# Kernel optimization log

Measured on AMD Instinct MI355X. Metric: run time of the kernel, lower is better.

## Reference

```python
import jax, jax.numpy as jnp
import numpy as np

N_DEST, N_SRC = 8192, 8192
FEAT, TFD, EMB, HID, HEADS = 1024, 256, 64, 128, 2
NEG_INF = -9e15


def setup_inputs() -> dict:
    key = jax.random.key(0)
    ks = jax.random.split(key, 8)
    bias = (jax.random.uniform(ks[0], (N_DEST, N_SRC)) < 0.01).astype(jnp.float32)
    emb_dest = jax.random.normal(ks[1], (N_DEST, EMB), jnp.float32)
    emb_src = jax.random.normal(ks[2], (N_SRC, EMB), jnp.float32)
    feature_src = jax.random.normal(ks[3], (N_SRC, FEAT), jnp.float32)
    scale = 0.05
    fc_W = jax.random.normal(ks[4], (TFD, FEAT), jnp.float32) * scale
    fc_b = jnp.zeros((TFD,), jnp.float32)
    dec_W = jax.random.normal(ks[5], (FEAT, TFD), jnp.float32) * scale
    dec_b = jnp.zeros((FEAT,), jnp.float32)
    att_W = jax.random.normal(ks[6], (HEADS, EMB, HID), jnp.float32) * scale
    att_W2 = jax.random.normal(ks[7], (HEADS, HID, HID), jnp.float32) * scale
    return dict(bias=bias, emb_dest=emb_dest, emb_src=emb_src,
                feature_src=feature_src, fc_W=fc_W, fc_b=fc_b,
                dec_W=dec_W, dec_b=dec_b, att_W=att_W, att_W2=att_W2)


def reference(bias, emb_dest, emb_src, feature_src, fc_W, fc_b, dec_W, dec_b, att_W, att_W2):
    # encoder: [N_src, FEAT] -> [N_src, TFD]
    transformed = feature_src @ fc_W.T + fc_b
    # per-head projections of node embeddings: h = emb @ W  -> [H, N, HID]
    h_src = jnp.einsum('ne,hed->hnd', emb_src, att_W)
    h_dst = jnp.einsum('me,hed->hmd', emb_dest, att_W)
    # e = elu((h_dst @ W2) @ h_src^T)  -> [H, N_dest, N_src]
    scores = jax.nn.elu(jnp.einsum('hmd,hdk,hnk->hmn', h_dst, att_W2, h_src))
    masked = jnp.where(bias > 0, scores, NEG_INF)
    attn = jax.nn.softmax(masked, axis=-1)  # row-wise over source nodes
    # aggregate transformed source features, mean over heads -> [N_dest, TFD]
    feature_src_re = jnp.einsum('hmn,nf->hmf', attn, transformed).mean(axis=0)
    # decoder (autoencoder reconstruction): [N_src, FEAT]
    feature_hat = transformed @ dec_W.T + dec_b
    return feature_src_re, feature_hat
```

## Files before the change

### kernel.cpp

```cpp
#include <hip/hip_runtime.h>
#include <hip/hip_bf16.h>

#define N_DEST 8192
#define N_SRC  8192
#define FEATD  1024
#define TFDIM  256
#define EMBD   64
#define HIDD   128
#define LDO    1024
#define SCAP 240
#define BMW  128

typedef float  f32x4  __attribute__((ext_vector_type(4)));
typedef __bf16 bf16x8 __attribute__((ext_vector_type(8)));
typedef unsigned short u16x4 __attribute__((ext_vector_type(4)));

__device__ inline bf16x8 load8cvt(const float* p) {
  const f32x4 u = *(const f32x4*)p;
  const f32x4 v = *(const f32x4*)(p + 4);
  bf16x8 r;
  #pragma unroll
  for (int i = 0; i < 4; ++i) { r[i] = (__bf16)u[i]; r[i + 4] = (__bf16)v[i]; }
  return r;
}
__device__ inline unsigned short bfbits(float f) {
  __bf16 b = (__bf16)f;
  return *(unsigned short*)&b;
}
__device__ inline float bf2f(unsigned short u) {
  union { unsigned int i; float f; } x;
  x.i = (unsigned int)u << 16;
  return x.f;
}

__global__ __launch_bounds__(256) void cvt_weights(
    const float* __restrict__ fc_W, const float* __restrict__ dec_W,
    unsigned short* __restrict__ wpack, unsigned short* __restrict__ dpack)
{
  const int which = blockIdx.x >> 8;
  const int i = ((blockIdx.x & 255) * 256 + threadIdx.x) * 4;
  const float* src = which ? dec_W : fc_W;
  unsigned short* dst = which ? dpack : wpack;
  const f32x4 v = *(const f32x4*)(src + i);
  u16x4 o;
  #pragma unroll
  for (int e = 0; e < 4; ++e) o[e] = bfbits(v[e]);
  *(u16x4*)(dst + i) = o;
}

__global__ __launch_bounds__(256) void bias_to_bits(
    const float* __restrict__ bias, unsigned long long* __restrict__ bm)
{
  const int m = blockIdx.x;
  const int tid = threadIdx.x, lane = tid & 63, wv = tid >> 6;
  const float* brow = bias + (size_t)m * N_SRC;
  unsigned long long* bmrow = bm + (size_t)m * BMW;
  #pragma unroll
  for (int k = 0; k < 8; ++k) {
    const f32x4 v = *(const f32x4*)(brow + k * 1024 + tid * 4);
    #pragma unroll
    for (int e = 0; e < 4; ++e) {
      const unsigned long long msk = __ballot(v[e] > 0.f);
      if (lane == 0) bmrow[k * 16 + wv * 4 + e] = msk;
    }
  }
}

__global__ __launch_bounds__(256) void gemm_mfma_k1(
    const float* __restrict__ A, const float* __restrict__ B,
    const float* __restrict__ bias, float* __restrict__ stage,
    unsigned short* __restrict__ apack,
    const unsigned short* __restrict__ wpack)
{
  const int wave = threadIdx.x >> 6, lane = threadIdx.x & 63;
  const int l15 = lane & 15, quad = lane >> 4;
  const int row0 = blockIdx.x * 64 + wave * 16;
  const int col0 = blockIdx.y * 64;

  const float* Ap = A + (size_t)(row0 + l15) * FEATD + quad * 8;

  f32x4 acc[4];
  #pragma unroll
  for (int i = 0; i < 4; ++i) acc[i] = (f32x4){0.f, 0.f, 0.f, 0.f};

  if (wpack) {
    const unsigned short* Bq = wpack + (size_t)(col0 + l15) * FEATD + quad * 8;
    for (int k = 0; k < FEATD; k += 32) {
      const bf16x8 a  = load8cvt(Ap + k);
      const bf16x8 b0 = *(const bf16x8*)(Bq + k);
      const bf16x8 b1 = *(const bf16x8*)(Bq + (size_t)16 * FEATD + k);
      const bf16x8 b2 = *(const bf16x8*)(Bq + (size_t)32 * FEATD + k);
      const bf16x8 b3 = *(const bf16x8*)(Bq + (size_t)48 * FEATD + k);
      acc[0] = __builtin_amdgcn_mfma_f32_16x16x32_bf16(a, b0, acc[0], 0, 0, 0);
      acc[1] = __builtin_amdgcn_mfma_f32_16x16x32_bf16(a, b1, acc[1], 0, 0, 0);
      acc[2] = __builtin_amdgcn_mfma_f32_16x16x32_bf16(a, b2, acc[2], 0, 0, 0);
      acc[3] = __builtin_amdgcn_mfma_f32_16x16x32_bf16(a, b3, acc[3], 0, 0, 0);
    }
  } else {
    const float* Bp = B + (size_t)(col0 + l15) * FEATD + quad * 8;
    for (int k = 0; k < FEATD; k += 32) {
      const bf16x8 a  = load8cvt(Ap + k);
      const bf16x8 b0 = load8cvt(Bp + k);
      const bf16x8 b1 = load8cvt(Bp + (size_t)16 * FEATD + k);
      const bf16x8 b2 = load8cvt(Bp + (size_t)32 * FEATD + k);
      const bf16x8 b3 = load8cvt(Bp + (size_t)48 * FEATD + k);
      acc[0] = __builtin_amdgcn_mfma_f32_16x16x32_bf16(a, b0, acc[0], 0, 0, 0);
      acc[1] = __builtin_amdgcn_mfma_f32_16x16x32_bf16(a, b1, acc[1], 0, 0, 0);
      acc[2] = __builtin_amdgcn_mfma_f32_16x16x32_bf16(a, b2, acc[2], 0, 0, 0);
      acc[3] = __builtin_amdgcn_mfma_f32_16x16x32_bf16(a, b3, acc[3], 0, 0, 0);
    }
  }

  #pragma unroll
  for (int ct = 0; ct < 4; ++ct) {
    const int n = col0 + ct * 16 + l15;
    const float bn = bias[n];
    #pragma unroll
    for (int r = 0; r < 4; ++r) {
      const int mm = row0 + quad * 4 + r;
      const float v = acc[ct][r] + bn;
      stage[(size_t)mm * LDO + n] = v;
      if (apack) apack[(size_t)mm * TFDIM + n] = bfbits(v);
    }
  }
}

__global__ __launch_bounds__(128) void proj_all(
    const float* __restrict__ emb_src, const float* __restrict__ emb_dest,
    const float* __restrict__ att_W, const float* __restrict__ att_W2,
    float* __restrict__ stage, unsigned short* __restrict__ hpack)
{
  const int t = threadIdx.x;
  const int b = blockIdx.x;
  const int rb    = b & 511;
  const int h     = (b >> 9) & 1;
  const int which = b >> 10;
  const int row0  = rb * 16;

  __shared__ float se[16][EMBD];
  __shared__ float hh[16][HIDD];

  const float* e = (which ? emb_dest : emb_src) + (size_t)row0 * EMBD;
  for (int i = t; i < 16 * EMBD; i += 128) se[i >> 6][i & 63] = e[i];
  __syncthreads();

  float acc[16];
  #pragma unroll
  for (int r = 0; r < 16; ++r) acc[r] = 0.f;
  const float* W = att_W + (size_t)h * EMBD * HIDD + t;
  for (int d = 0; d < EMBD; ++d) {
    const float w = W[d * HIDD];
    #pragma unroll
    for (int r = 0; r < 16; ++r) acc[r] += se[r][d] * w;
  }

  if (!which) {
    #pragma unroll
    for (int r = 0; r < 16; ++r) {
      const size_t row = row0 + r;
      stage[row * LDO + 256 + h * HIDD + t] = acc[r];
      if (hpack) hpack[row * TFDIM + h * HIDD + t] = bfbits(acc[r]);
    }
    return;
  }

  #pragma unroll
  for (int r = 0; r < 16; ++r) hh[r][t] = acc[r];
  __syncthreads();

  float g[16];
  #pragma unroll
  for (int r = 0; r < 16; ++r) g[r] = 0.f;
  const float* W2 = att_W2 + (size_t)h * HIDD * HIDD + t;
  for (int d = 0; d < HIDD; ++d) {
    const float w2 = W2[d * HIDD];
    #pragma unroll
    for (int r = 0; r < 16; ++r) g[r] += hh[r][d] * w2;
  }
  #pragma unroll
  for (int r = 0; r < 16; ++r)
    stage[(size_t)(row0 + r) * LDO + 512 + h * HIDD + t] = g[r];
}

__global__ __launch_bounds__(256, 6) void attn_fused(
    const unsigned long long* __restrict__ bm, const float* __restrict__ stage,
    const unsigned short* __restrict__ hpack,
    const unsigned short* __restrict__ apack,
    float* __restrict__ out)
{
  const int m = blockIdx.x;
  const int tid = threadIdx.x;
  const int lane = tid & 63, wv = tid >> 6;

  __shared__ float gq[4][68];
  __shared__ unsigned long long bmw[BMW];
  __shared__ float s0[256], s1[256];
  __shared__ int   lidx[256];
  __shared__ float rA[4], rB[4];
  __shared__ float p0[4][TFDIM], p1[4][TFDIM];
  __shared__ int   cnt;

  const float* gs = stage + (size_t)m * LDO + 512;
  gq[wv][lane] = gs[(wv >> 1) * HIDD + (wv & 1) * 64 + lane];
  if (tid < BMW) bmw[tid] = bm[(size_t)m * BMW + tid];
  if (tid == 0) cnt = 0;
  __syncthreads();

  int wcount = 0;
  if (lane < 32) wcount = __popcll(bmw[(lane >> 2) * 16 + wv * 4 + (lane & 3)]);
  #pragma unroll
  for (int off = 32; off; off >>= 1) wcount += __shfl_xor(wcount, off);
  int wbase = 0;
  if (lane == 0) wbase = atomicAdd(&cnt, wcount);
  wbase = __shfl(wbase, 0);

  int off = wbase;
  #pragma unroll
  for (int k = 0; k < 8; ++k) {
    #pragma unroll
    for (int e = 0; e < 4; ++e) {
      const unsigned long long msk = bmw[k * 16 + wv * 4 + e];
      if ((msk >> lane) & 1ull) {
        const int p = off + __popcll(msk & ((1ull << lane) - 1ull));
        if (p < 256) lidx[p] = k * 1024 + wv * 256 + lane * 4 + e;
      }
      off += __popcll(msk);
    }
  }
  __syncthreads();
  const int count = cnt;

  if (count > 0 && count <= SCAP) {
    const int countPad = (count + 15) & ~15;
    if (tid >= count && tid < countPad) lidx[tid] = 0;
    __syncthreads();

    const int grp = tid >> 2, r4 = tid & 3;
    const int h = r4 >> 1, half = r4 & 1;
    const float* gh = gq[r4];
    for (int t0 = 0; t0 < count; t0 += 64) {
      const int t = t0 + grp;
      float q = 0.f;
      if (t < count) {
        const int j = lidx[t];
        const __bf16* hb =
            (const __bf16*)hpack + (size_t)j * TFDIM + h * HIDD + half * 64;
        #pragma unroll
        for (int s = 0; s < 8; ++s) {
          const bf16x8 x = *(const bf16x8*)(hb + s * 8);
          #pragma unroll
          for (int e = 0; e < 8; ++e) q += gh[s * 8 + e] * (float)x[e];
        }
      }
      q += __shfl_xor(q, 1);
      if (t < count && half == 0) {
        const float sc = (q > 0.f) ? q : expm1f(q);
        if (h == 0) s0[t] = sc; else s1[t] = sc;
      }
    }
    __syncthreads();

    float m0 = (tid < count) ? s0[tid] : -3.4e38f;
    float m1 = (tid < count) ? s1[tid] : -3.4e38f;
    #pragma unroll
    for (int o = 32; o; o >>= 1) {
      m0 = fmaxf(m0, __shfl_xor(m0, o));
      m1 = fmaxf(m1, __shfl_xor(m1, o));
    }
    if (lane == 0) { rA[wv] = m0; rB[wv] = m1; }
    __syncthreads();
    const float M0 = fmaxf(fmaxf(rA[0], rA[1]), fmaxf(rA[2], rA[3]));
    const float M1 = fmaxf(fmaxf(rB[0], rB[1]), fmaxf(rB[2], rB[3]));
    __syncthreads();

    float w0 = 0.f, w1 = 0.f;
    if (tid < count) {
      w0 = __expf(s0[tid] - M0);
      w1 = __expf(s1[tid] - M1);
    }
    if (tid < countPad) { s0[tid] = w0; s1[tid] = w1; }
    float l0 = w0, l1 = w1;
    #pragma unroll
    for (int o = 32; o; o >>= 1) {
      l0 += __shfl_xor(l0, o);
      l1 += __shfl_xor(l1, o);
    }
    if (lane == 0) { rA[wv] = l0; rB[wv] = l1; }
    __syncthreads();
    const float L0 = rA[0] + rA[1] + rA[2] + rA[3];
    const float L1 = rB[0] + rB[1] + rB[2] + rB[3];

    float b0[4] = {0.f, 0.f, 0.f, 0.f};
    float b1[4] = {0.f, 0.f, 0.f, 0.f};
    const int c4 = lane << 2;
    for (int t = wv << 2; t < countPad; t += 16) {
      #pragma unroll
      for (int q = 0; q < 4; ++q) {
        const int j = lidx[t + q];
        const float u0 = s0[t + q], u1 = s1[t + q];
        const u16x4 tv = *(const u16x4*)(apack + (size_t)j * TFDIM + c4);
        #pragma unroll
        for (int i = 0; i < 4; ++i) {
          const float f = bf2f(tv[i]);
          b0[i] += u0 * f;
          b1[i] += u1 * f;
        }
      }
    }
    #pragma unroll
    for (int i = 0; i < 4; ++i) {
      p0[wv][c4 + i] = b0[i];
      p1[wv][c4 + i] = b1[i];
    }
    __syncthreads();
    const float A0 = p0[0][tid] + p0[1][tid] + p0[2][tid] + p0[3][tid];
    const float A1 = p1[0][tid] + p1[1][tid] + p1[2][tid] + p1[3][tid];
    out[(size_t)m * TFDIM + tid] = 0.5f * (A0 / L0 + A1 / L1);
    return;
  }

  float* w0s = (float*)p0[0];
  float* w1s = (float*)p0[1];
  const int c = tid;
  float a0 = 0.f, a1 = 0.f;
  float M0 = -3.4e38f, M1 = -3.4e38f, L0 = 0.f, L1 = 0.f;
  for (int j0 = 0; j0 < N_SRC; j0 += 256) {
    const int j = j0 + tid;
    const float* hb = stage + (size_t)j * LDO + 256;
    float q0 = 0.f, q1 = 0.f;
    for (int d = 0; d < HIDD; d += 4) {
      const int hf = d >> 6, dd = d & 63;
      const f32x4 x = *(const f32x4*)(hb + d);
      const f32x4 y = *(const f32x4*)(hb + HIDD + d);
      #pragma unroll
      for (int e = 0; e < 4; ++e) {
        q0 += gq[hf][dd + e] * x[e];
        q1 += gq[2 + hf][dd + e] * y[e];
      }
    }
    const int kk = j >> 10, rr = j & 1023;
    const int wq = rr >> 8, ll = (rr & 255) >> 2, ee = rr & 3;
    const bool nz = (bmw[kk * 16 + wq * 4 + ee] >> ll) & 1ull;
    const float sc0 = nz ? ((q0 > 0.f) ? q0 : expm1f(q0)) : -9e15f;
    const float sc1 = nz ? ((q1 > 0.f) ? q1 : expm1f(q1)) : -9e15f;

    float cm0 = sc0, cm1 = sc1;
    #pragma unroll
    for (int o = 32; o; o >>= 1) {
      cm0 = fmaxf(cm0, __shfl_xor(cm0, o));
      cm1 = fmaxf(cm1, __shfl_xor(cm1, o));
    }
    if (lane == 0) { rA[wv] = cm0; rB[wv] = cm1; }
    __syncthreads();
    const float CM0 = fmaxf(fmaxf(rA[0], rA[1]), fmaxf(rA[2], rA[3]));
    const float CM1 = fmaxf(fmaxf(rB[0], rB[1]), fmaxf(rB[2], rB[3]));
    __syncthreads();

    const float nM0 = fmaxf(M0, CM0), nM1 = fmaxf(M1, CM1);
    const float r0 = __expf(M0 - nM0), r1 = __expf(M1 - nM1);
    const float w0 = __expf(sc0 - nM0), w1 = __expf(sc1 - nM1);
    w0s[tid] = w0; w1s[tid] = w1;
    float cl0 = w0, cl1 = w1;
    #pragma unroll
    for (int o = 32; o; o >>= 1) {
      cl0 += __shfl_xor(cl0, o);
      cl1 += __shfl_xor(cl1, o);
    }
    if (lane == 0) { rA[wv] = cl0; rB[wv] = cl1; }
    __syncthreads();
    L0 = L0 * r0 + (rA[0] + rA[1] + rA[2] + rA[3]);
    L1 = L1 * r1 + (rB[0] + rB[1] + rB[2] + rB[3]);
    M0 = nM0; M1 = nM1;
    a0 *= r0; a1 *= r1;
    for (int t2 = 0; t2 < 256; ++t2) {
      const float tv = stage[(size_t)(j0 + t2) * LDO + c];
      a0 += w0s[t2] * tv;
      a1 += w1s[t2] * tv;
    }
    __syncthreads();
  }
  out[(size_t)m * TFDIM + c] = 0.5f * (a0 / L0 + a1 / L1);
}

__global__ __launch_bounds__(64) void attn_stream(
    const float* __restrict__ bias, const float* __restrict__ stage,
    float* __restrict__ out)
{
  const int lane = threadIdx.x;
  const int m = blockIdx.x;
  const int c0 = lane * 4;

  __shared__ float g0[HIDD], g1[HIDD];
  __shared__ int   ring[256];
  __shared__ float wb0[64], wb1[64];

  const float* gs = stage + (size_t)m * LDO + 512;
  g0[lane]      = gs[lane];
  g0[lane + 64] = gs[lane + 64];
  g1[lane]      = gs[HIDD + lane];
  g1[lane + 64] = gs[HIDD + lane + 64];
  __syncthreads();

  float O0[4] = {0.f, 0.f, 0.f, 0.f};
  float O1[4] = {0.f, 0.f, 0.f, 0.f};
  float M0 = -3.4e38f, M1 = -3.4e38f;
  float L0 = 0.f, L1 = 0.f;

  auto flush = [&](int b, int rp) {
    __syncthreads();
    int j = -1;
    if (lane < b) j = ring[(rp + lane) & 255];
    float s0 = 0.f, s1 = 0.f;
    if (j >= 0) {
      const float* h0 = stage + (size_t)j * LDO + 256;
      const float* h1 = h0 + HIDD;
      #pragma unroll
      for (int d = 0; d < HIDD; d += 4) {
        const f32x4 a = *(const f32x4*)(h0 + d);
        const f32x4 c = *(const f32x4*)(h1 + d);
        #pragma unroll
        for (int e = 0; e < 4; ++e) {
          s0 += g0[d + e] * a[e];
          s1 += g1[d + e] * c[e];
        }
      }
      s0 = (s0 > 0.f) ? s0 : expm1f(s0);
      s1 = (s1 > 0.f) ? s1 : expm1f(s1);
    }
    float m0 = (j >= 0) ? s0 : -3.4e38f;
    float m1 = (j >= 0) ? s1 : -3.4e38f;
    #pragma unroll
    for (int off = 32; off; off >>= 1) {
      m0 = fmaxf(m0, __shfl_xor(m0, off));
      m1 = fmaxf(m1, __shfl_xor(m1, off));
    }
    const float nM0 = fmaxf(M0, m0), nM1 = fmaxf(M1, m1);
    const float w0 = (j >= 0) ? __expf(s0 - nM0) : 0.f;
    const float w1 = (j >= 0) ? __expf(s1 - nM1) : 0.f;
    float l0 = w0, l1 = w1;
    #pragma unroll
    for (int off = 32; off; off >>= 1) {
      l0 += __shfl_xor(l0, off);
      l1 += __shfl_xor(l1, off);
    }
    const float r0 = __expf(M0 - nM0);
    const float r1 = __expf(M1 - nM1);
    L0 = L0 * r0 + l0;  L1 = L1 * r1 + l1;
    M0 = nM0;  M1 = nM1;
    #pragma unroll
    for (int i = 0; i < 4; ++i) { O0[i] *= r0; O1[i] *= r1; }
    wb0[lane] = w0;  wb1[lane] = w1;
    __syncthreads();
    for (int n = 0; n < b; ++n) {
      const int jj = ring[(rp + n) & 255];
      const float wa = wb0[n], wc = wb1[n];
      const f32x4 tv = *(const f32x4*)(stage + (size_t)jj * LDO + c0);
      #pragma unroll
      for (int i = 0; i < 4; ++i) {
        O0[i] += wa * tv[i];
        O1[i] += wc * tv[i];
      }
    }
    __syncthreads();
  };

  const float* brow = bias + (size_t)m * N_SRC;
  int wpos = 0, rpos = 0;
  for (int base = 0; base < N_SRC; base += 256) {
    const f32x4 v = *(const f32x4*)(brow + base + lane * 4);
    #pragma unroll
    for (int e = 0; e < 4; ++e) {
      const bool nz = v[e] > 0.f;
      const unsigned long long mask = __ballot(nz);
      if (nz) {
        const int pos = wpos + __popcll(mask & ((1ull << lane) - 1ull));
        ring[pos & 255] = base + lane * 4 + e;
      }
      wpos += __popcll(mask);
      if (wpos - rpos >= 64) { flush(64, rpos); rpos += 64; }
    }
  }
  while (wpos - rpos > 0) {
    const int b = (wpos - rpos < 64) ? (wpos - rpos) : 64;
    flush(b, rpos);
    rpos += b;
  }

  float* orow = out + (size_t)m * TFDIM + c0;
  if (wpos == 0) {
    float o[4] = {0.f, 0.f, 0.f, 0.f};
    for (int j = 0; j < N_SRC; ++j) {
      const f32x4 tv = *(const f32x4*)(stage + (size_t)j * LDO + c0);
      #pragma unroll
      for (int i = 0; i < 4; ++i) o[i] += tv[i];
    }
    const float inv = 1.f / (float)N_SRC;
    #pragma unroll
    for (int i = 0; i < 4; ++i) orow[i] = o[i] * inv;
  } else {
    const float i0 = 1.f / L0, i1 = 1.f / L1;
    #pragma unroll
    for (int i = 0; i < 4; ++i)
      orow[i] = 0.5f * (O0[i] * i0 + O1[i] * i1);
  }
}

__global__ __launch_bounds__(256) void gemm_mfma_dec2(
    const unsigned short* __restrict__ apack,
    const unsigned short* __restrict__ dpack,
    const float* __restrict__ bias,
    float* __restrict__ OUT)
{
  const int wave = threadIdx.x >> 6, lane = threadIdx.x & 63;
  const int l15 = lane & 15, quad = lane >> 4;
  const int row0 = blockIdx.x * 64 + wave * 16;
  const int col0 = blockIdx.y * 64;

  const unsigned short* Ap = apack + (size_t)(row0 + l15) * TFDIM + quad * 8;
  const unsigned short* Bp = dpack + (size_t)(col0 + l15) * TFDIM + quad * 8;

  f32x4 acc[4];
  #pragma unroll
  for (int i = 0; i < 4; ++i) acc[i] = (f32x4){0.f, 0.f, 0.f, 0.f};

  #pragma unroll
  for (int k = 0; k < TFDIM; k += 32) {
    const bf16x8 a  = *(const bf16x8*)(Ap + k);
    const bf16x8 b0 = *(const bf16x8*)(Bp + k);
    const bf16x8 b1 = *(const bf16x8*)(Bp + (size_t)16 * TFDIM + k);
    const bf16x8 b2 = *(const bf16x8*)(Bp + (size_t)32 * TFDIM + k);
    const bf16x8 b3 = *(const bf16x8*)(Bp + (size_t)48 * TFDIM + k);
    acc[0] = __builtin_amdgcn_mfma_f32_16x16x32_bf16(a, b0, acc[0], 0, 0, 0);
    acc[1] = __builtin_amdgcn_mfma_f32_16x16x32_bf16(a, b1, acc[1], 0, 0, 0);
    acc[2] = __builtin_amdgcn_mfma_f32_16x16x32_bf16(a, b2, acc[2], 0, 0, 0);
    acc[3] = __builtin_amdgcn_mfma_f32_16x16x32_bf16(a, b3, acc[3], 0, 0, 0);
  }

  #pragma unroll
  for (int ct = 0; ct < 4; ++ct) {
    const int n = col0 + ct * 16 + l15;
    const float bn = bias[n];
    #pragma unroll
    for (int r = 0; r < 4; ++r) {
      const int mm = row0 + quad * 4 + r;
      OUT[(size_t)mm * LDO + n] = acc[ct][r] + bn;
    }
  }
}

__global__ __launch_bounds__(128) void gemm_mfma_dec(
    const float* __restrict__ W,
    const float* __restrict__ bias,
    float* __restrict__ OUT)
{
  const int row0 = blockIdx.x * 32;
  const int tid = threadIdx.x;
  const int wave = tid >> 6, lane = tid & 63;
  const int l15 = lane & 15, quad = lane >> 4;

  __shared__ __bf16 Ab[32][TFDIM + 8];

  for (int i = tid; i < 32 * TFDIM; i += 128) {
    const int r = i >> 8, k = i & 255;
    Ab[r][k] = (__bf16)OUT[(size_t)(row0 + r) * LDO + k];
  }
  __syncthreads();

  bf16x8 af[8];
  #pragma unroll
  for (int ks = 0; ks < 8; ++ks)
    af[ks] = *(const bf16x8*)&Ab[wave * 16 + l15][ks * 32 + quad * 8];

  for (int ct = 0; ct < 16; ++ct) {
    f32x4 acc[4];
    #pragma unroll
    for (int i = 0; i < 4; ++i) acc[i] = (f32x4){0.f, 0.f, 0.f, 0.f};
    #pragma unroll
    for (int ks = 0; ks < 8; ++ks) {
      #pragma unroll
      for (int cg = 0; cg < 4; ++cg) {
        const int n = ct * 64 + cg * 16 + l15;
        const bf16x8 bf = load8cvt(W + (size_t)n * TFDIM + ks * 32 + quad * 8);
        acc[cg] = __builtin_amdgcn_mfma_f32_16x16x32_bf16(af[ks], bf, acc[cg], 0, 0, 0);
      }
    }
    #pragma unroll
    for (int cg = 0; cg < 4; ++cg) {
      const int n = ct * 64 + cg * 16 + l15;
      const float bn = bias[n];
      #pragma unroll
      for (int r = 0; r < 4; ++r) {
        const int mm = row0 + wave * 16 + quad * 4 + r;
        OUT[(size_t)mm * LDO + n] = acc[cg][r] + bn;
      }
    }
  }
}

extern "C" void kernel_launch(void* const* d_in, const int* in_sizes, int n_in,
                              void* d_out, int out_size, void* d_ws, size_t ws_size,
                              hipStream_t stream) {
  const float* bias        = (const float*)d_in[0];
  const float* emb_dest    = (const float*)d_in[1];
  const float* emb_src     = (const float*)d_in[2];
  const float* feature_src = (const float*)d_in[3];
  const float* fc_W        = (const float*)d_in[4];
  const float* fc_b        = (const float*)d_in[5];
  const float* dec_W       = (const float*)d_in[6];
  const float* dec_b       = (const float*)d_in[7];
  const float* att_W       = (const float*)d_in[8];
  const float* att_W2      = (const float*)d_in[9];

  float* out0 = (float*)d_out;
  float* out1 = out0 + (size_t)N_DEST * TFDIM;

  const size_t apack_bytes = (size_t)N_SRC * TFDIM * sizeof(unsigned short);
  const size_t wpack_bytes = (size_t)TFDIM * FEATD * sizeof(unsigned short);
  const size_t dpack_bytes = (size_t)FEATD * TFDIM * sizeof(unsigned short);
  const size_t hpack_bytes = (size_t)N_SRC * TFDIM * sizeof(unsigned short);
  const size_t bm_bytes    = (size_t)N_DEST * BMW * sizeof(unsigned long long);
  const bool use_ws = (ws_size >=
      apack_bytes + wpack_bytes + dpack_bytes + hpack_bytes + bm_bytes);
  unsigned short* apack = (unsigned short*)d_ws;
  unsigned short* wpack = (unsigned short*)((char*)d_ws + apack_bytes);
  unsigned short* dpack = (unsigned short*)((char*)wpack + wpack_bytes);
  unsigned short* hpack = (unsigned short*)((char*)dpack + dpack_bytes);
  unsigned long long* bm =
      (unsigned long long*)((char*)hpack + hpack_bytes);

  if (use_ws) {
    cvt_weights<<<512, 256, 0, stream>>>(fc_W, dec_W, wpack, dpack);
    bias_to_bits<<<N_DEST, 256, 0, stream>>>(bias, bm);
  }

  {
    dim3 grid(N_SRC / 64, TFDIM / 64);
    gemm_mfma_k1<<<grid, 256, 0, stream>>>(
        feature_src, fc_W, fc_b, out1,
        use_ws ? apack : (unsigned short*)nullptr,
        use_ws ? wpack : (const unsigned short*)nullptr);
  }
  proj_all<<<2048, 128, 0, stream>>>(emb_src, emb_dest, att_W, att_W2, out1,
                                     use_ws ? hpack : (unsigned short*)nullptr);
  if (use_ws) {
    attn_fused<<<N_DEST, 256, 0, stream>>>(bm, out1, hpack, apack, out0);
  } else {
    attn_stream<<<N_DEST, 64, 0, stream>>>(bias, out1, out0);
  }
  if (use_ws) {
    dim3 grid(N_SRC / 64, FEATD / 64);
    gemm_mfma_dec2<<<grid, 256, 0, stream>>>(apack, dpack, dec_b, out1);
  } else {
    gemm_mfma_dec<<<N_SRC / 32, 128, 0, stream>>>(dec_W, dec_b, out1);
  }
}
```

Measured before the change: 658.6 us.

## Fuse bias bitmask scan into one-wave-per-row attention kernel

```diff
diff --git a/kernel.cpp b/kernel.cpp
--- a/kernel.cpp
+++ b/kernel.cpp
@@ -9,7 +9,6 @@
 #define HIDD   128
 #define LDO    1024
 #define SCAP 240
-#define BMW  128
 
 typedef float  f32x4  __attribute__((ext_vector_type(4)));
 typedef __bf16 bf16x8 __attribute__((ext_vector_type(8)));
@@ -46,24 +45,6 @@
   #pragma unroll
   for (int e = 0; e < 4; ++e) o[e] = bfbits(v[e]);
   *(u16x4*)(dst + i) = o;
-}
-
-__global__ __launch_bounds__(256) void bias_to_bits(
-    const float* __restrict__ bias, unsigned long long* __restrict__ bm)
-{
-  const int m = blockIdx.x;
-  const int tid = threadIdx.x, lane = tid & 63, wv = tid >> 6;
-  const float* brow = bias + (size_t)m * N_SRC;
-  unsigned long long* bmrow = bm + (size_t)m * BMW;
-  #pragma unroll
-  for (int k = 0; k < 8; ++k) {
-    const f32x4 v = *(const f32x4*)(brow + k * 1024 + tid * 4);
-    #pragma unroll
-    for (int e = 0; e < 4; ++e) {
-      const unsigned long long msk = __ballot(v[e] > 0.f);
-      if (lane == 0) bmrow[k * 16 + wv * 4 + e] = msk;
-    }
-  }
 }
 
 __global__ __launch_bounds__(256) void gemm_mfma_k1(
@@ -119,8 +100,8 @@
     for (int r = 0; r < 4; ++r) {
       const int mm = row0 + quad * 4 + r;
       const float v = acc[ct][r] + bn;
-      stage[(size_t)mm * LDO + n] = v;
       if (apack) apack[(size_t)mm * TFDIM + n] = bfbits(v);
+      else       stage[(size_t)mm * LDO + n] = v;
     }
   }
 }
@@ -158,8 +139,8 @@
     #pragma unroll
     for (int r = 0; r < 16; ++r) {
       const size_t row = row0 + r;
-      stage[row * LDO + 256 + h * HIDD + t] = acc[r];
       if (hpack) hpack[row * TFDIM + h * HIDD + t] = bfbits(acc[r]);
+      else       stage[row * LDO + 256 + h * HIDD + t] = acc[r];
     }
     return;
   }
@@ -182,67 +163,58 @@
     stage[(size_t)(row0 + r) * LDO + 512 + h * HIDD + t] = g[r];
 }
 
-__global__ __launch_bounds__(256, 6) void attn_fused(
-    const unsigned long long* __restrict__ bm, const float* __restrict__ stage,
+__global__ __launch_bounds__(256, 6) void attn_wave(
+    const float* __restrict__ bias, const float* __restrict__ stage,
     const unsigned short* __restrict__ hpack,
     const unsigned short* __restrict__ apack,
     float* __restrict__ out)
 {
-  const int m = blockIdx.x;
-  const int tid = threadIdx.x;
-  const int lane = tid & 63, wv = tid >> 6;
-
-  __shared__ float gq[4][68];
-  __shared__ unsigned long long bmw[BMW];
-  __shared__ float s0[256], s1[256];
-  __shared__ int   lidx[256];
-  __shared__ float rA[4], rB[4];
-  __shared__ float p0[4][TFDIM], p1[4][TFDIM];
-  __shared__ int   cnt;
+  const int wv = threadIdx.x >> 6, lane = threadIdx.x & 63;
+  const int m = blockIdx.x * 4 + wv;
+
+  __shared__ float gq[4][4][68];
+  __shared__ float s0[4][256], s1[4][256];
+  __shared__ int   lidx[4][256];
 
   const float* gs = stage + (size_t)m * LDO + 512;
-  gq[wv][lane] = gs[(wv >> 1) * HIDD + (wv & 1) * 64 + lane];
-  if (tid < BMW) bmw[tid] = bm[(size_t)m * BMW + tid];
-  if (tid == 0) cnt = 0;
-  __syncthreads();
-
-  int wcount = 0;
-  if (lane < 32) wcount = __popcll(bmw[(lane >> 2) * 16 + wv * 4 + (lane & 3)]);
-  #pragma unroll
-  for (int off = 32; off; off >>= 1) wcount += __shfl_xor(wcount, off);
-  int wbase = 0;
-  if (lane == 0) wbase = atomicAdd(&cnt, wcount);
-  wbase = __shfl(wbase, 0);
-
-  int off = wbase;
-  #pragma unroll
-  for (int k = 0; k < 8; ++k) {
+  {
+    const f32x4 gv = *(const f32x4*)(gs + lane * 4);
+    #pragma unroll
+    for (int i = 0; i < 4; ++i) {
+      const int idx = lane * 4 + i;
+      gq[wv][idx >> 6][idx & 63] = gv[i];
+    }
+  }
+
+  const float* brow = bias + (size_t)m * N_SRC;
+  int off = 0;
+  for (int r = 0; r < 32; ++r) {
+    const f32x4 v = *(const f32x4*)(brow + r * 256 + lane * 4);
     #pragma unroll
     for (int e = 0; e < 4; ++e) {
-      const unsigned long long msk = bmw[k * 16 + wv * 4 + e];
-      if ((msk >> lane) & 1ull) {
+      const bool nz = v[e] > 0.f;
+      const unsigned long long msk = __ballot(nz);
+      if (nz) {
         const int p = off + __popcll(msk & ((1ull << lane) - 1ull));
-        if (p < 256) lidx[p] = k * 1024 + wv * 256 + lane * 4 + e;
+        if (p < 256) lidx[wv][p] = r * 256 + lane * 4 + e;
       }
       off += __popcll(msk);
     }
   }
-  __syncthreads();
-  const int count = cnt;
+  const int count = off;
 
   if (count > 0 && count <= SCAP) {
-    const int countPad = (count + 15) & ~15;
-    if (tid >= count && tid < countPad) lidx[tid] = 0;
-    __syncthreads();
-
-    const int grp = tid >> 2, r4 = tid & 3;
+    const int countPad = (count + 3) & ~3;
+    if (lane < countPad - count) lidx[wv][count + lane] = 0;
+
+    const int grp = lane >> 2, r4 = lane & 3;
     const int h = r4 >> 1, half = r4 & 1;
-    const float* gh = gq[r4];
-    for (int t0 = 0; t0 < count; t0 += 64) {
+    const float* gh = gq[wv][r4];
+    for (int t0 = 0; t0 < count; t0 += 16) {
       const int t = t0 + grp;
       float q = 0.f;
       if (t < count) {
-        const int j = lidx[t];
+        const int j = lidx[wv][t];
         const __bf16* hb =
             (const __bf16*)hpack + (size_t)j * TFDIM + h * HIDD + half * 64;
         #pragma unroll
@@ -255,49 +227,45 @@
       q += __shfl_xor(q, 1);
       if (t < count && half == 0) {
         const float sc = (q > 0.f) ? q : expm1f(q);
-        if (h == 0) s0[t] = sc; else s1[t] = sc;
-      }
-    }
-    __syncthreads();
-
-    float m0 = (tid < count) ? s0[tid] : -3.4e38f;
-    float m1 = (tid < count) ? s1[tid] : -3.4e38f;
+        if (h == 0) s0[wv][t] = sc; else s1[wv][t] = sc;
+      }
+    }
+
+    float m0 = -3.4e38f, m1 = -3.4e38f;
+    for (int t = lane; t < count; t += 64) {
+      m0 = fmaxf(m0, s0[wv][t]);
+      m1 = fmaxf(m1, s1[wv][t]);
+    }
     #pragma unroll
     for (int o = 32; o; o >>= 1) {
       m0 = fmaxf(m0, __shfl_xor(m0, o));
       m1 = fmaxf(m1, __shfl_xor(m1, o));
     }
-    if (lane == 0) { rA[wv] = m0; rB[wv] = m1; }
-    __syncthreads();
-    const float M0 = fmaxf(fmaxf(rA[0], rA[1]), fmaxf(rA[2], rA[3]));
-    const float M1 = fmaxf(fmaxf(rB[0], rB[1]), fmaxf(rB[2], rB[3]));
-    __syncthreads();
-
-    float w0 = 0.f, w1 = 0.f;
-    if (tid < count) {
-      w0 = __expf(s0[tid] - M0);
-      w1 = __expf(s1[tid] - M1);
-    }
-    if (tid < countPad) { s0[tid] = w0; s1[tid] = w1; }
-    float l0 = w0, l1 = w1;
+
+    float l0 = 0.f, l1 = 0.f;
+    for (int t = lane; t < countPad; t += 64) {
+      float w0 = 0.f, w1 = 0.f;
+      if (t < count) {
+        w0 = __expf(s0[wv][t] - m0);
+        w1 = __expf(s1[wv][t] - m1);
+      }
+      s0[wv][t] = w0; s1[wv][t] = w1;
+      l0 += w0; l1 += w1;
+    }
     #pragma unroll
     for (int o = 32; o; o >>= 1) {
       l0 += __shfl_xor(l0, o);
       l1 += __shfl_xor(l1, o);
     }
-    if (lane == 0) { rA[wv] = l0; rB[wv] = l1; }
-    __syncthreads();
-    const float L0 = rA[0] + rA[1] + rA[2] + rA[3];
-    const float L1 = rB[0] + rB[1] + rB[2] + rB[3];
 
     float b0[4] = {0.f, 0.f, 0.f, 0.f};
     float b1[4] = {0.f, 0.f, 0.f, 0.f};
     const int c4 = lane << 2;
-    for (int t = wv << 2; t < countPad; t += 16) {
+    for (int t = 0; t < countPad; t += 4) {
       #pragma unroll
       for (int q = 0; q < 4; ++q) {
-        const int j = lidx[t + q];
-        const float u0 = s0[t + q], u1 = s1[t + q];
+        const int j = lidx[wv][t + q];
+        const float u0 = s0[wv][t + q], u1 = s1[wv][t + q];
         const u16x4 tv = *(const u16x4*)(apack + (size_t)j * TFDIM + c4);
         #pragma unroll
         for (int i = 0; i < 4; ++i) {
@@ -307,40 +275,33 @@
         }
       }
     }
-    #pragma unroll
-    for (int i = 0; i < 4; ++i) {
-      p0[wv][c4 + i] = b0[i];
-      p1[wv][c4 + i] = b1[i];
-    }
-    __syncthreads();
-    const float A0 = p0[0][tid] + p0[1][tid] + p0[2][tid] + p0[3][tid];
-    const float A1 = p1[0][tid] + p1[1][tid] + p1[2][tid] + p1[3][tid];
-    out[(size_t)m * TFDIM + tid] = 0.5f * (A0 / L0 + A1 / L1);
+    float* orow = out + (size_t)m * TFDIM + c4;
+    #pragma unroll
+    for (int i = 0; i < 4; ++i)
+      orow[i] = 0.5f * (b0[i] / l0 + b1[i] / l1);
     return;
   }
 
-  float* w0s = (float*)p0[0];
-  float* w1s = (float*)p0[1];
-  const int c = tid;
-  float a0 = 0.f, a1 = 0.f;
   float M0 = -3.4e38f, M1 = -3.4e38f, L0 = 0.f, L1 = 0.f;
-  for (int j0 = 0; j0 < N_SRC; j0 += 256) {
-    const int j = j0 + tid;
-    const float* hb = stage + (size_t)j * LDO + 256;
+  float a0[4] = {0.f, 0.f, 0.f, 0.f};
+  float a1[4] = {0.f, 0.f, 0.f, 0.f};
+  const int c4 = lane << 2;
+  for (int j0 = 0; j0 < N_SRC; j0 += 64) {
+    const int j = j0 + lane;
+    const __bf16* hb = (const __bf16*)hpack + (size_t)j * TFDIM;
     float q0 = 0.f, q1 = 0.f;
-    for (int d = 0; d < HIDD; d += 4) {
-      const int hf = d >> 6, dd = d & 63;
-      const f32x4 x = *(const f32x4*)(hb + d);
-      const f32x4 y = *(const f32x4*)(hb + HIDD + d);
-      #pragma unroll
-      for (int e = 0; e < 4; ++e) {
-        q0 += gq[hf][dd + e] * x[e];
-        q1 += gq[2 + hf][dd + e] * y[e];
-      }
-    }
-    const int kk = j >> 10, rr = j & 1023;
-    const int wq = rr >> 8, ll = (rr & 255) >> 2, ee = rr & 3;
-    const bool nz = (bmw[kk * 16 + wq * 4 + ee] >> ll) & 1ull;
+    #pragma unroll
+    for (int s = 0; s < 16; ++s) {
+      const bf16x8 x = *(const bf16x8*)(hb + s * 8);
+      const bf16x8 y = *(const bf16x8*)(hb + HIDD + s * 8);
+      #pragma unroll
+      for (int e = 0; e < 8; ++e) {
+        const int d = s * 8 + e;
+        q0 += gq[wv][d >> 6][d & 63] * (float)x[e];
+        q1 += gq[wv][2 + (d >> 6)][d & 63] * (float)y[e];
+      }
+    }
+    const bool nz = brow[j] > 0.f;
     const float sc0 = nz ? ((q0 > 0.f) ? q0 : expm1f(q0)) : -9e15f;
     const float sc1 = nz ? ((q1 > 0.f) ? q1 : expm1f(q1)) : -9e15f;
 
@@ -350,36 +311,35 @@
       cm0 = fmaxf(cm0, __shfl_xor(cm0, o));
       cm1 = fmaxf(cm1, __shfl_xor(cm1, o));
     }
-    if (lane == 0) { rA[wv] = cm0; rB[wv] = cm1; }
-    __syncthreads();
-    const float CM0 = fmaxf(fmaxf(rA[0], rA[1]), fmaxf(rA[2], rA[3]));
-    const float CM1 = fmaxf(fmaxf(rB[0], rB[1]), fmaxf(rB[2], rB[3]));
-    __syncthreads();
-
-    const float nM0 = fmaxf(M0, CM0), nM1 = fmaxf(M1, CM1);
+    const float nM0 = fmaxf(M0, cm0), nM1 = fmaxf(M1, cm1);
     const float r0 = __expf(M0 - nM0), r1 = __expf(M1 - nM1);
     const float w0 = __expf(sc0 - nM0), w1 = __expf(sc1 - nM1);
-    w0s[tid] = w0; w1s[tid] = w1;
+    s0[wv][lane] = w0; s1[wv][lane] = w1;
     float cl0 = w0, cl1 = w1;
     #pragma unroll
     for (int o = 32; o; o >>= 1) {
       cl0 += __shfl_xor(cl0, o);
       cl1 += __shfl_xor(cl1, o);
     }
-    if (lane == 0) { rA[wv] = cl0; rB[wv] = cl1; }
-    __syncthreads();
-    L0 = L0 * r0 + (rA[0] + rA[1] + rA[2] + rA[3]);
-    L1 = L1 * r1 + (rB[0] + rB[1] + rB[2] + rB[3]);
+    L0 = L0 * r0 + cl0;  L1 = L1 * r1 + cl1;
     M0 = nM0; M1 = nM1;
-    a0 *= r0; a1 *= r1;
-    for (int t2 = 0; t2 < 256; ++t2) {
-      const float tv = stage[(size_t)(j0 + t2) * LDO + c];
-      a0 += w0s[t2] * tv;
-      a1 += w1s[t2] * tv;
-    }
-    __syncthreads();
-  }
-  out[(size_t)m * TFDIM + c] = 0.5f * (a0 / L0 + a1 / L1);
+    #pragma unroll
+    for (int i = 0; i < 4; ++i) { a0[i] *= r0; a1[i] *= r1; }
+    for (int n = 0; n < 64; ++n) {
+      const float u0 = s0[wv][n], u1 = s1[wv][n];
+      const u16x4 tv = *(const u16x4*)(apack + (size_t)(j0 + n) * TFDIM + c4);
+      #pragma unroll
+      for (int i = 0; i < 4; ++i) {
+        const float f = bf2f(tv[i]);
+        a0[i] += u0 * f;
+        a1[i] += u1 * f;
+      }
+    }
+  }
+  float* orow = out + (size_t)m * TFDIM + c4;
+  #pragma unroll
+  for (int i = 0; i < 4; ++i)
+    orow[i] = 0.5f * (a0[i] / L0 + a1[i] / L1);
 }
 
 __global__ __launch_bounds__(64) void attn_stream(
@@ -618,20 +578,15 @@
   const size_t wpack_bytes = (size_t)TFDIM * FEATD * sizeof(unsigned short);
   const size_t dpack_bytes = (size_t)FEATD * TFDIM * sizeof(unsigned short);
   const size_t hpack_bytes = (size_t)N_SRC * TFDIM * sizeof(unsigned short);
-  const size_t bm_bytes    = (size_t)N_DEST * BMW * sizeof(unsigned long long);
-  const bool use_ws = (ws_size >=
-      apack_bytes + wpack_bytes + dpack_bytes + hpack_bytes + bm_bytes);
+  const bool use_ws =
+      (ws_size >= apack_bytes + wpack_bytes + dpack_bytes + hpack_bytes);
   unsigned short* apack = (unsigned short*)d_ws;
   unsigned short* wpack = (unsigned short*)((char*)d_ws + apack_bytes);
   unsigned short* dpack = (unsigned short*)((char*)wpack + wpack_bytes);
   unsigned short* hpack = (unsigned short*)((char*)dpack + dpack_bytes);
-  unsigned long long* bm =
-      (unsigned long long*)((char*)hpack + hpack_bytes);
-
-  if (use_ws) {
+
+  if (use_ws)
     cvt_weights<<<512, 256, 0, stream>>>(fc_W, dec_W, wpack, dpack);
-    bias_to_bits<<<N_DEST, 256, 0, stream>>>(bias, bm);
-  }
 
   {
     dim3 grid(N_SRC / 64, TFDIM / 64);
@@ -643,7 +598,7 @@
   proj_all<<<2048, 128, 0, stream>>>(emb_src, emb_dest, att_W, att_W2, out1,
                                      use_ws ? hpack : (unsigned short*)nullptr);
   if (use_ws) {
-    attn_fused<<<N_DEST, 256, 0, stream>>>(bm, out1, hpack, apack, out0);
+    attn_wave<<<N_DEST / 4, 256, 0, stream>>>(bias, out1, hpack, apack, out0);
   } else {
     attn_stream<<<N_DEST, 64, 0, stream>>>(bias, out1, out0);
   }
```

Result: slower. 675.7 us (+2.6%).
